# Optimization experiments

Hardware: AMD Instinct MI355X
Metric: run time of the kernel (lower is better)

The kernel has to match this reference:

```python
import jax, jax.numpy as jnp
import numpy as np

CONFUSED_PAIRS = [(1, 2), (3, 4), (5, 6)]
NUM_CLASSES = 13
MARGIN = 0.5
IGNORE_INDEX = -100
BIG = 1e9  # finite sentinel instead of +/-inf (keeps grads clean)
EPS = 1e-12  # matches F.normalize eps

_conf_np = np.zeros((NUM_CLASSES, NUM_CLASSES), dtype=bool)
for _a, _b in CONFUSED_PAIRS:
    _conf_np[_a, _b] = True
    _conf_np[_b, _a] = True
CONF = jnp.asarray(_conf_np)  # [C, C] symmetric confused-class table


def setup_inputs() -> dict:
    key = jax.random.key(0)
    k1, k2 = jax.random.split(key)
    embeddings = jax.random.normal(k1, (16, 512, 256), dtype=jnp.float32)
    labels = jax.random.randint(k2, (16, 512), 0, 13, dtype=jnp.int64)
    return {"embeddings": embeddings, "labels": labels}


def reference(embeddings, labels):
    B, S, H = embeddings.shape
    e = embeddings.reshape(-1, H)                      # [N, H]
    lab = labels.reshape(-1)                           # [N]
    N = e.shape[0]

    valid = lab != IGNORE_INDEX                        # [N]
    # L2 normalize (F.normalize: divide by norm clamped to eps)
    norm = jnp.linalg.norm(e, axis=1, keepdims=True)
    e = e / jnp.maximum(norm, EPS)

    sim = e @ e.T                                      # [N, N] cosine sims

    lab_c = jnp.clip(lab, 0, NUM_CLASSES - 1)          # safe gather index
    # anchor label participates in some confused pair, and anchor is valid
    anchor_ok = valid & CONF[lab_c].any(axis=1)        # [N]

    same = lab[:, None] == lab[None, :]                # [N, N]
    eye = jnp.eye(N, dtype=bool)
    pos_mask = same & valid[None, :] & ~eye            # positives: same class, not self
    neg_mask = CONF[lab_c[:, None], lab_c[None, :]] & valid[None, :]  # confused-class negatives

    has_pos = pos_mask.any(axis=1)
    has_neg = neg_mask.any(axis=1)
    count_mask = anchor_ok & has_pos & has_neg         # [N] anchors contributing a triplet

    hardest_pos = jnp.min(jnp.where(pos_mask, sim, BIG), axis=1)   # [N]
    hardest_neg = jnp.max(jnp.where(neg_mask, sim, -BIG), axis=1)  # [N]

    triplet = jax.nn.relu(MARGIN + hardest_neg - hardest_pos)
    triplet = jnp.where(count_mask, triplet, 0.0)

    num_triplets = count_mask.sum()
    loss = triplet.sum() / jnp.maximum(num_triplets, 1).astype(triplet.dtype)
    return jnp.where(num_triplets > 0, loss, 0.0)
```

## Files before the change

kernel.cpp:

```cpp
#include <hip/hip_runtime.h>
#include <math.h>

#define Hdim    256
#define NMAX    8192
#define NPADMAX (NMAX + 6 * 32)
#define WLMAX   264
#define BIGV    1e9f
#define MARGIN  0.5f

typedef __attribute__((ext_vector_type(8))) short bf16x8;
typedef __attribute__((ext_vector_type(4))) float f32x4;

struct WS {
    unsigned short ebf[NPADMAX][Hdim];
    int gpos[NMAX];
    int S[8];
    int n[8];
    int wl_a[WLMAX];
    int wl_c[WLMAX];
    int T;
    unsigned done;
    float wsum;
    int   wcnt;
};

__device__ inline unsigned short f2bf(float f) {
    unsigned u = __float_as_uint(f);
    return (unsigned short)((u + 0x7fffu + ((u >> 16) & 1u)) >> 16);
}

__global__ __launch_bounds__(1024) void plan_kernel(const int* __restrict__ lab,
                                                    WS* ws, int N) {
    __shared__ int h[8];
    __shared__ int S[8];
    __shared__ int cur[8];
    const int tid = threadIdx.x;
    if (tid < 8) h[tid] = 0;
    __syncthreads();
    for (int i = tid; i < N; i += 1024) {
        int l = lab[i];
        if (l >= 1 && l <= 6) atomicAdd(&h[l], 1);
    }
    __syncthreads();
    if (tid == 0) {
        int acc = 0;
        for (int c = 1; c <= 6; ++c) { S[c] = acc; acc += ((h[c] + 31) >> 5) << 5; }
        S[0] = 0; S[7] = acc;
        int T = 0;
        for (int c = 1; c <= 6; ++c) {
            int nt = (h[c] + 31) >> 5;
            for (int k = 0; k < nt; ++k) { ws->wl_a[T] = S[c] + 32 * k; ws->wl_c[T] = c; ++T; }
        }
        ws->T = T;
        ws->done = 0u; ws->wsum = 0.f; ws->wcnt = 0;
        for (int c = 0; c < 8; ++c) { ws->n[c] = h[c]; ws->S[c] = S[c]; }
    }
    __syncthreads();
    if (tid < 8) cur[tid] = S[tid];
    __syncthreads();
    for (int i = tid; i < N; i += 1024) {
        int l = lab[i];
        ws->gpos[i] = (l >= 1 && l <= 6) ? atomicAdd(&cur[l], 1) : -1;
    }
}

__global__ __launch_bounds__(256) void norm_gather_kernel(const float* __restrict__ in,
                                                          WS* ws) {
    int row  = blockIdx.x * 4 + (threadIdx.x >> 6);
    int lane = threadIdx.x & 63;
    int g = ws->gpos[row];
    if (g < 0) return;
    float4 v = ((const float4*)(in + (size_t)row * Hdim))[lane];
    float ss = v.x*v.x + v.y*v.y + v.z*v.z + v.w*v.w;
    #pragma unroll
    for (int off = 32; off >= 1; off >>= 1) ss += __shfl_xor(ss, off);
    float sc = 1.0f / fmaxf(sqrtf(ss), 1e-12f);
    ushort4 o;
    o.x = f2bf(v.x * sc); o.y = f2bf(v.y * sc);
    o.z = f2bf(v.z * sc); o.w = f2bf(v.w * sc);
    ((ushort4*)(&ws->ebf[g][0]))[lane] = o;
}

__global__ __launch_bounds__(256) void sim_kernel(WS* ws, float* __restrict__ out) {
    const int wave = threadIdx.x >> 6;
    const int lane = threadIdx.x & 63;
    const int col  = lane & 15;
    const int quad = lane >> 4;
    const int tileIdx = blockIdx.x;

    __shared__ float lds_hp[4][32], lds_hn[4][32];

    if (tileIdx < ws->T) {
        const int aBase = ws->wl_a[tileIdx];
        const int c     = ws->wl_c[tileIdx];
        const int p     = ((c - 1) ^ 1) + 1;
        const int posS = ws->S[c], posRealE = posS + ws->n[c];
        const int negS = ws->S[p], negRealE = negS + ws->n[p];
        const int nPosT = (ws->S[c + 1] - posS) >> 4;
        const int nNegT = (ws->S[p + 1] - negS) >> 4;
        const int nTT   = nPosT + nNegT;
        const bool hasPN = (ws->n[c] >= 2) && (ws->n[p] >= 1);

        const unsigned short* ebf = &ws->ebf[0][0];

        bf16x8 afrag[2][8];
        #pragma unroll
        for (int t2 = 0; t2 < 2; ++t2) {
            const unsigned short* rp = ebf + (size_t)(aBase + t2 * 16 + col) * Hdim + quad * 8;
            #pragma unroll
            for (int ks = 0; ks < 8; ++ks)
                afrag[t2][ks] = *(const bf16x8*)(rp + ks * 32);
        }

        float runMin[2][4], runMax[2][4];
        #pragma unroll
        for (int t2 = 0; t2 < 2; ++t2)
            #pragma unroll
            for (int r = 0; r < 4; ++r) { runMin[t2][r] = BIGV; runMax[t2][r] = -BIGV; }

        auto j0Of = [&](int t) -> int {
            return (t < nPosT) ? (posS + (t << 4)) : (negS + ((t - nPosT) << 4));
        };
        bf16x8 b0[8], b1[8];
        auto loadB = [&](bf16x8 (&bf)[8], int t) {
            const unsigned short* rp = ebf + (size_t)(j0Of(t) + col) * Hdim + quad * 8;
            #pragma unroll
            for (int ks = 0; ks < 8; ++ks)
                bf[ks] = *(const bf16x8*)(rp + ks * 32);
        };
        auto computeT = [&](bf16x8 (&bf)[8], int t) {
            int j0 = j0Of(t);
            bool isPos = t < nPosT;
            int realE  = isPos ? posRealE : negRealE;
            bool valid = (j0 + col) < realE;
            #pragma unroll
            for (int t2 = 0; t2 < 2; ++t2) {
                f32x4 acc = {0.f, 0.f, 0.f, 0.f};
                #pragma unroll
                for (int ks = 0; ks < 8; ++ks)
                    acc = __builtin_amdgcn_mfma_f32_16x16x32_bf16(afrag[t2][ks], bf[ks], acc, 0, 0, 0);
                if (isPos) {
                    #pragma unroll
                    for (int r = 0; r < 4; ++r)
                        runMin[t2][r] = fminf(runMin[t2][r], valid ? acc[r] : BIGV);
                } else {
                    #pragma unroll
                    for (int r = 0; r < 4; ++r)
                        runMax[t2][r] = fmaxf(runMax[t2][r], valid ? acc[r] : -BIGV);
                }
            }
        };

        int nIter = (nTT > wave) ? ((nTT - wave + 3) >> 2) : 0;
        int t = wave, i = 0;
        if (nIter > 0) loadB(b0, t);
        while (i + 2 <= nIter) {
            loadB(b1, t + 4);
            computeT(b0, t);
            if (i + 2 < nIter) loadB(b0, t + 8);
            computeT(b1, t + 4);
            t += 8; i += 2;
        }
        if (i < nIter) computeT(b0, t);

        #pragma unroll
        for (int t2 = 0; t2 < 2; ++t2)
            #pragma unroll
            for (int r = 0; r < 4; ++r) {
                float mn = runMin[t2][r], mx = runMax[t2][r];
                #pragma unroll
                for (int off = 1; off < 16; off <<= 1) {
                    mn = fminf(mn, __shfl_xor(mn, off));
                    mx = fmaxf(mx, __shfl_xor(mx, off));
                }
                if (col == 0) {
                    int a = t2 * 16 + quad * 4 + r;
                    lds_hp[wave][a] = mn;
                    lds_hn[wave][a] = mx;
                }
            }
        __syncthreads();

        if (wave == 0) {
            float contrib = 0.f; int cc = 0;
            if (lane < 32) {
                float hp = fminf(fminf(lds_hp[0][lane], lds_hp[1][lane]),
                                 fminf(lds_hp[2][lane], lds_hp[3][lane]));
                float hn = fmaxf(fmaxf(lds_hn[0][lane], lds_hn[1][lane]),
                                 fmaxf(lds_hn[2][lane], lds_hn[3][lane]));
                bool real = (aBase + lane) < posRealE;
                if (real && hasPN) {
                    float tr = MARGIN + hn - hp;
                    contrib = (tr > 0.f) ? tr : 0.f;
                    cc = 1;
                }
            }
            #pragma unroll
            for (int off = 32; off >= 1; off >>= 1) {
                contrib += __shfl_xor(contrib, off);
                cc      += __shfl_xor(cc, off);
            }
            if (lane == 0) {
                atomicAdd(&ws->wsum, contrib);
                atomicAdd(&ws->wcnt, cc);
            }
        }
    }

    if (threadIdx.x == 0) {
        __builtin_amdgcn_s_waitcnt(0);
        unsigned old = atomicAdd(&ws->done, 1u);
        if (old == (unsigned)(gridDim.x - 1)) {
            float s = atomicAdd(&ws->wsum, 0.0f);
            int   n = atomicAdd(&ws->wcnt, 0);
            out[0] = (n > 0) ? s / (float)n : 0.f;
        }
    }
}

extern "C" void kernel_launch(void* const* d_in, const int* in_sizes, int n_in,
                              void* d_out, int out_size, void* d_ws, size_t ws_size,
                              hipStream_t stream) {
    const float* emb = (const float*)d_in[0];
    const int*   lab = (const int*)d_in[1];
    int N = in_sizes[1];
    WS* ws = (WS*)d_ws;

    plan_kernel<<<1, 1024, 0, stream>>>(lab, ws, N);
    norm_gather_kernel<<<(N + 3) / 4, 256, 0, stream>>>(emb, ws);
    sim_kernel<<<WLMAX, 256, 0, stream>>>(ws, (float*)d_out);
}
```

Baseline: 95.11 us.

## Fuse label planning and normalize-gather into one multi-block prep kernel

Replaces the single-block plan kernel and the separate normalize/gather kernel with one prep kernel. Each block redundantly counts the labels, computes per-class prefix offsets for its 32 rows, and assigns compacted positions with ballot/popcount instead of atomics. This removes one launch, the serial single-block histogram pass, and the gpos round trip through global memory. In exchange every block rescans all N labels, and ordering within a class is now deterministic rather than set by atomics.

```diff
diff --git a/kernel.cpp b/kernel.cpp
--- a/kernel.cpp
+++ b/kernel.cpp
@@ -13,7 +13,6 @@
 
 struct WS {
     unsigned short ebf[NPADMAX][Hdim];
-    int gpos[NMAX];
     int S[8];
     int n[8];
     int wl_a[WLMAX];
@@ -29,56 +28,83 @@
     return (unsigned short)((u + 0x7fffu + ((u >> 16) & 1u)) >> 16);
 }
 
-__global__ __launch_bounds__(1024) void plan_kernel(const int* __restrict__ lab,
-                                                    WS* ws, int N) {
-    __shared__ int h[8];
-    __shared__ int S[8];
-    __shared__ int cur[8];
-    const int tid = threadIdx.x;
-    if (tid < 8) h[tid] = 0;
+__global__ __launch_bounds__(256) void prep_kernel(const float* __restrict__ in,
+                                                   const int* __restrict__ lab,
+                                                   WS* ws, int N) {
+    const int b    = blockIdx.x;
+    const int tid  = threadIdx.x;
+    const int wave = tid >> 6, lane = tid & 63;
+    const int r0   = b * 32;
+
+    int cAll[6] = {0,0,0,0,0,0}, cPre[6] = {0,0,0,0,0,0};
+    for (int j = tid; j < N; j += 256) {
+        int l = lab[j];
+        int pre = (j < r0);
+        #pragma unroll
+        for (int c = 0; c < 6; ++c) {
+            int m = (l == c + 1);
+            cAll[c] += m;
+            cPre[c] += m & pre;
+        }
+    }
+    __shared__ int sAll[4][6], sPre[4][6];
+    #pragma unroll
+    for (int c = 0; c < 6; ++c) {
+        int a = cAll[c], p2 = cPre[c];
+        #pragma unroll
+        for (int off = 32; off >= 1; off >>= 1) { a += __shfl_xor(a, off); p2 += __shfl_xor(p2, off); }
+        if (lane == 0) { sAll[wave][c] = a; sPre[wave][c] = p2; }
+    }
     __syncthreads();
-    for (int i = tid; i < N; i += 1024) {
-        int l = lab[i];
-        if (l >= 1 && l <= 6) atomicAdd(&h[l], 1);
+    __shared__ int S[8], P[8], gArr[32];
+    if (tid == 0) {
+        int acc = 0; S[0] = 0;
+        for (int c = 1; c <= 6; ++c) {
+            int h  = sAll[0][c-1] + sAll[1][c-1] + sAll[2][c-1] + sAll[3][c-1];
+            int pr = sPre[0][c-1] + sPre[1][c-1] + sPre[2][c-1] + sPre[3][c-1];
+            S[c] = acc; P[c] = pr;
+            acc += ((h + 31) >> 5) << 5;
+        }
+        S[7] = acc;
     }
     __syncthreads();
-    if (tid == 0) {
-        int acc = 0;
-        for (int c = 1; c <= 6; ++c) { S[c] = acc; acc += ((h[c] + 31) >> 5) << 5; }
-        S[0] = 0; S[7] = acc;
+    if (wave == 0) {
+        int l = (lane < 32) ? lab[r0 + lane] : 0;
+        int g = -1;
+        #pragma unroll
+        for (int c = 1; c <= 6; ++c) {
+            unsigned long long mask = __ballot(l == c);
+            if (l == c) g = S[c] + P[c] + __popcll(mask & ((1ULL << lane) - 1ULL));
+        }
+        if (lane < 32) gArr[lane] = g;
+    }
+    __syncthreads();
+    for (int k = wave; k < 32; k += 4) {
+        int g = gArr[k];
+        if (g < 0) continue;
+        int row = r0 + k;
+        float4 v = ((const float4*)(in + (size_t)row * Hdim))[lane];
+        float ss = v.x*v.x + v.y*v.y + v.z*v.z + v.w*v.w;
+        #pragma unroll
+        for (int off = 32; off >= 1; off >>= 1) ss += __shfl_xor(ss, off);
+        float sc = 1.0f / fmaxf(sqrtf(ss), 1e-12f);
+        ushort4 o;
+        o.x = f2bf(v.x * sc); o.y = f2bf(v.y * sc);
+        o.z = f2bf(v.z * sc); o.w = f2bf(v.w * sc);
+        ((ushort4*)(&ws->ebf[g][0]))[lane] = o;
+    }
+    if (b == 0 && tid == 0) {
         int T = 0;
         for (int c = 1; c <= 6; ++c) {
-            int nt = (h[c] + 31) >> 5;
-            for (int k = 0; k < nt; ++k) { ws->wl_a[T] = S[c] + 32 * k; ws->wl_c[T] = c; ++T; }
-        }
+            int h = sAll[0][c-1] + sAll[1][c-1] + sAll[2][c-1] + sAll[3][c-1];
+            ws->n[c] = h; ws->S[c] = S[c];
+            int nt = (h + 31) >> 5;
+            for (int kk = 0; kk < nt; ++kk) { ws->wl_a[T] = S[c] + 32 * kk; ws->wl_c[T] = c; ++T; }
+        }
+        ws->n[0] = 0; ws->n[7] = 0; ws->S[0] = 0; ws->S[7] = S[7];
         ws->T = T;
         ws->done = 0u; ws->wsum = 0.f; ws->wcnt = 0;
-        for (int c = 0; c < 8; ++c) { ws->n[c] = h[c]; ws->S[c] = S[c]; }
-    }
-    __syncthreads();
-    if (tid < 8) cur[tid] = S[tid];
-    __syncthreads();
-    for (int i = tid; i < N; i += 1024) {
-        int l = lab[i];
-        ws->gpos[i] = (l >= 1 && l <= 6) ? atomicAdd(&cur[l], 1) : -1;
-    }
-}
-
-__global__ __launch_bounds__(256) void norm_gather_kernel(const float* __restrict__ in,
-                                                          WS* ws) {
-    int row  = blockIdx.x * 4 + (threadIdx.x >> 6);
-    int lane = threadIdx.x & 63;
-    int g = ws->gpos[row];
-    if (g < 0) return;
-    float4 v = ((const float4*)(in + (size_t)row * Hdim))[lane];
-    float ss = v.x*v.x + v.y*v.y + v.z*v.z + v.w*v.w;
-    #pragma unroll
-    for (int off = 32; off >= 1; off >>= 1) ss += __shfl_xor(ss, off);
-    float sc = 1.0f / fmaxf(sqrtf(ss), 1e-12f);
-    ushort4 o;
-    o.x = f2bf(v.x * sc); o.y = f2bf(v.y * sc);
-    o.z = f2bf(v.z * sc); o.w = f2bf(v.w * sc);
-    ((ushort4*)(&ws->ebf[g][0]))[lane] = o;
+    }
 }
 
 __global__ __launch_bounds__(256) void sim_kernel(WS* ws, float* __restrict__ out) {
@@ -226,7 +252,6 @@
     int N = in_sizes[1];
     WS* ws = (WS*)d_ws;
 
-    plan_kernel<<<1, 1024, 0, stream>>>(lab, ws, N);
-    norm_gather_kernel<<<(N + 3) / 4, 256, 0, stream>>>(emb, ws);
+    prep_kernel<<<N / 32, 256, 0, stream>>>(emb, lab, ws, N);
     sim_kernel<<<WLMAX, 256, 0, stream>>>(ws, (float*)d_out);
 }
```

Measured after the change: 104.4 us. 9.8% more time.
